# Kernel optimization log

Hardware: AMD Instinct MI355X
Metric: run time of the kernel (lower is better)

The kernel has to match this reference:

```python
import jax, jax.numpy as jnp
import numpy as np

# Wrapped module: Linear(2048->8192) + ReLU + Linear(8192->2048), both with bias.
D_IN, D_FF, D_OUT = 2048, 8192, 2048
N_W1 = D_FF * D_IN
N_B1 = D_FF
N_W2 = D_OUT * D_FF
N_B2 = D_OUT
NUM_WANDB = N_W1 + N_B1 + N_W2 + N_B2  # 33,564,672
SIZE_N = 5794  # ceil(sqrt(NUM_WANDB))
SIZE_M = 2897  # ceil(1.0 * SIZE_N / 2)
BATCH = 4096


def setup_inputs() -> dict:
    key = jax.random.key(0)
    k1, k2, k3 = jax.random.split(key, 3)
    x = jax.random.normal(k1, (BATCH, D_IN), dtype=jnp.float32)
    # scale factors keep reconstructed weights in a sane numeric range
    V1 = jax.random.normal(k2, (SIZE_N, SIZE_M), dtype=jnp.float32) * 0.02
    V2 = jax.random.normal(k3, (SIZE_N, SIZE_M), dtype=jnp.float32) * 0.02
    return {"x": x, "V1": V1, "V2": V2}


def reference(x, V1, V2):
    # V = V1 @ V2^T, flattened row-major (matches torch .view(-1, 1))
    V = jnp.matmul(V1, V2.T).reshape(-1)
    # Vectorized equivalent of WandBtoV's per-element copy loop:
    # consecutive slices of V fill each weight/bias in named_modules order.
    o = 0
    W1 = V[o:o + N_W1].reshape(D_FF, D_IN); o += N_W1   # linear1.weight [out,in]
    b1 = V[o:o + N_B1]; o += N_B1                        # linear1.bias
    W2 = V[o:o + N_W2].reshape(D_OUT, D_FF); o += N_W2   # linear2.weight
    b2 = V[o:o + N_B2]                                   # linear2.bias
    h = jax.nn.relu(jnp.matmul(x, W1.T) + b1)            # [B, D_FF]
    return jnp.matmul(h, W2.T) + b2                      # [B, D_OUT]
```

## Files before the change

### kernel.cpp

```cpp
#include <hip/hip_runtime.h>
#include <hip/hip_bf16.h>

typedef __attribute__((ext_vector_type(8))) __bf16 bf16x8;
typedef __attribute__((ext_vector_type(4))) __bf16 bf16x4;
typedef __attribute__((ext_vector_type(16))) float f32x16;

#define D_IN   2048
#define D_FF   8192
#define D_OUT  2048
#define BATCH  4096
#define SIZE_N 5794
#define SIZE_M 2897
#define PN 5888
#define PK 2944

#define OFF_B1 16777216
#define OFF_W2 16785408
#define OFF_B2 33562624

#define BK   32
#define NBUF 4

__device__ __forceinline__ void gload_lds16(const __bf16* g, __bf16* lds) {
    __builtin_amdgcn_global_load_lds(
        (const __attribute__((address_space(1))) void*)g,
        (__attribute__((address_space(3))) void*)lds,
        16, 0, 0);
}

template<int N> __device__ __forceinline__ void wait_vmcnt() {
    static_assert(N == 0 || N == 3 || N == 4 || N == 6 || N == 8, "unsupported vmcnt");
    if constexpr (N == 0)      asm volatile("s_waitcnt vmcnt(0)" ::: "memory");
    else if constexpr (N == 3) asm volatile("s_waitcnt vmcnt(3)" ::: "memory");
    else if constexpr (N == 4) asm volatile("s_waitcnt vmcnt(4)" ::: "memory");
    else if constexpr (N == 6) asm volatile("s_waitcnt vmcnt(6)" ::: "memory");
    else                       asm volatile("s_waitcnt vmcnt(8)" ::: "memory");
}
__device__ __forceinline__ void wait_lgkm0() {
    asm volatile("s_waitcnt lgkmcnt(0)" ::: "memory");
}

template<int MODE, int BM, int BN>
__global__ __launch_bounds__(512, 2)
void gemm_nt2(const __bf16* __restrict__ A, int lda,
              const __bf16* __restrict__ B, int ldb,
              void* __restrict__ Cv, int ldc,
              const __bf16* __restrict__ bias,
              int K, int Mvalid, int Nvalid)
{
    constexpr int LA = BM / 128;
    constexpr int LB = BN / 128;
    constexpr int L  = LA + LB;
    constexpr int FM = BM / 64;
    constexpr int FN = BN / 128;
    constexpr int ROWS = BM + BN;

    __shared__ bf16x8 lds[NBUF * ROWS * 4];

    const int tid  = threadIdx.x;
    const int wave = tid >> 6;
    const int lane = tid & 63;

    const int bm0 = blockIdx.x * BM;
    const int bn0 = blockIdx.y * BN;

    const int wm = wave >> 2;
    const int wn = wave & 3;

    const int srow   = lane >> 2;
    const int schunk = ((lane & 3) ^ ((lane >> 3) & 3)) * 8;

    const __bf16* aS = A + (size_t)(bm0 + wave * (BM / 8) + srow) * lda + schunk;
    const __bf16* bS = B + (size_t)(bn0 + wave * (BN / 8) + srow) * ldb + schunk;

    auto stage = [&](int t) {
        const int bb = t & (NBUF - 1);
        bf16x8* bufA = &lds[bb * ROWS * 4];
        bf16x8* bufB = bufA + BM * 4;
        const size_t kof = (size_t)t * BK;
        #pragma unroll
        for (int i = 0; i < LA; ++i)
            gload_lds16(aS + kof + (size_t)(16 * i) * lda,
                        (__bf16*)&bufA[(wave * (BM / 8) + 16 * i) * 4]);
        #pragma unroll
        for (int i = 0; i < LB; ++i)
            gload_lds16(bS + kof + (size_t)(16 * i) * ldb,
                        (__bf16*)&bufB[(wave * (BN / 8) + 16 * i) * 4]);
    };

    const int fr  = lane & 31;
    const int kh  = lane >> 5;
    const int swz = (fr >> 1) & 3;

    f32x16 acc[FM][FN] = {};

    const int nt = K / BK;

    stage(0); stage(1); stage(2);
    wait_vmcnt<2 * L>();
    __builtin_amdgcn_s_barrier();

    for (int t = 0; t < nt; ++t) {
        if (t + 3 < nt) stage(t + 3);

        const int bb = t & (NBUF - 1);
        const bf16x8* bufA = &lds[bb * ROWS * 4];
        const bf16x8* bufB = bufA + BM * 4;

        #pragma unroll
        for (int ks = 0; ks < 2; ++ks) {
            const int sl = (2 * ks + kh) ^ swz;
            bf16x8 af[FM], bq[FN];
            #pragma unroll
            for (int m = 0; m < FM; ++m)
                af[m] = bufA[(wm * (BM / 2) + m * 32 + fr) * 4 + sl];
            #pragma unroll
            for (int n = 0; n < FN; ++n)
                bq[n] = bufB[(wn * (BN / 4) + n * 32 + fr) * 4 + sl];
            __builtin_amdgcn_s_setprio(1);
            #pragma unroll
            for (int m = 0; m < FM; ++m) {
                #pragma unroll
                for (int n = 0; n < FN; ++n)
                    acc[m][n] = __builtin_amdgcn_mfma_f32_32x32x16_bf16(
                        af[m], bq[n], acc[m][n], 0, 0, 0);
            }
            __builtin_amdgcn_s_setprio(0);
        }

        if (t + 1 < nt) {
            wait_lgkm0();
            if      (t + 3 < nt) wait_vmcnt<2 * L>();
            else if (t + 2 < nt) wait_vmcnt<L>();
            else                 wait_vmcnt<0>();
            __builtin_amdgcn_s_barrier();
        }
    }

    const int ecol = lane & 31;
    const int er0  = 4 * kh;
    #pragma unroll
    for (int m = 0; m < FM; ++m) {
        #pragma unroll
        for (int n = 0; n < FN; ++n) {
            const int colBase = bn0 + wn * (BN / 4) + n * 32 + ecol;
            #pragma unroll
            for (int reg = 0; reg < 16; ++reg) {
                const int row = bm0 + wm * (BM / 2) + m * 32
                              + (reg & 3) + 8 * (reg >> 2) + er0;
                float v = acc[m][n][reg];
                if constexpr (MODE == 0) {
                    if (row < Mvalid && colBase < Nvalid)
                        ((__bf16*)Cv)[(size_t)row * ldc + colBase] = (__bf16)v;
                } else if constexpr (MODE == 1) {
                    v += (float)bias[colBase];
                    v = v > 0.f ? v : 0.f;
                    ((__bf16*)Cv)[(size_t)row * ldc + colBase] = (__bf16)v;
                } else {
                    v += (float)bias[colBase];
                    ((float*)Cv)[(size_t)row * ldc + colBase] = v;
                }
            }
        }
    }
}

__global__ void pad_cvt_bf16(const float* __restrict__ in, __bf16* __restrict__ out,
                             int rows, int cols, int pcols, int total)
{
    int idx = blockIdx.x * blockDim.x + threadIdx.x;
    if (idx >= total) return;
    int r = idx / pcols;
    int c = idx - r * pcols;
    float v = (r < rows && c < cols) ? in[(size_t)r * cols + c] : 0.0f;
    out[idx] = (__bf16)v;
}

__global__ void cvt_bf16_vec(const float4* __restrict__ in, bf16x4* __restrict__ out, int n4)
{
    int i = blockIdx.x * blockDim.x + threadIdx.x;
    if (i >= n4) return;
    float4 v = in[i];
    bf16x4 o;
    o.x = (__bf16)v.x; o.y = (__bf16)v.y; o.z = (__bf16)v.z; o.w = (__bf16)v.w;
    out[i] = o;
}

extern "C" void kernel_launch(void* const* d_in, const int* in_sizes, int n_in,
                              void* d_out, int out_size, void* d_ws, size_t ws_size,
                              hipStream_t stream)
{
    const float* x  = (const float*)d_in[0];
    const float* V1 = (const float*)d_in[1];
    const float* V2 = (const float*)d_in[2];
    float* out = (float*)d_out;

    char* ws = (char*)d_ws;
    const size_t vbElems  = (size_t)SIZE_N * SIZE_N;
    const size_t padElems = (size_t)PN * PK;

    size_t off = 0;
    __bf16* Vb = (__bf16*)(ws + off);
    off += ((vbElems * 2 + 255) / 256) * 256;
    __bf16* V1b = (__bf16*)(ws + off);
    __bf16* V2b = V1b + padElems;
    __bf16* hb  = (__bf16*)(ws + off);
    off += ((2 * padElems * 2 + 255) / 256) * 256;
    __bf16* xb = (__bf16*)(ws + off);
    off += (size_t)BATCH * D_IN * 2;
    if (ws_size < off) return;

    {
        int total  = (int)padElems;
        int blocks = (total + 255) / 256;
        pad_cvt_bf16<<<blocks, 256, 0, stream>>>(V1, V1b, SIZE_N, SIZE_M, PK, total);
        pad_cvt_bf16<<<blocks, 256, 0, stream>>>(V2, V2b, SIZE_N, SIZE_M, PK, total);
        int n4 = BATCH * D_IN / 4;
        cvt_bf16_vec<<<(n4 + 255) / 256, 256, 0, stream>>>((const float4*)x, (bf16x4*)xb, n4);
    }

    gemm_nt2<0, 256, 256><<<dim3(PN / 256, PN / 256), 512, 0, stream>>>(
        V1b, PK, V2b, PK, (void*)Vb, SIZE_N, (const __bf16*)nullptr, PK, SIZE_N, SIZE_N);

    gemm_nt2<1, 256, 256><<<dim3(BATCH / 256, D_FF / 256), 512, 0, stream>>>(
        xb, D_IN, Vb, D_IN, (void*)hb, D_FF, Vb + OFF_B1, D_IN, BATCH, D_FF);

    gemm_nt2<2, 128, 256><<<dim3(BATCH / 128, D_OUT / 256), 512, 0, stream>>>(
        hb, D_FF, Vb + OFF_W2, D_FF, (void*)out, D_OUT, Vb + OFF_B2, D_FF, BATCH, D_OUT);
}
```

Measured before the change: 780.0 us.

## Rework GEMM pipeline to 3-stage split A/B staging with smaller tiles

Replaces the GEMM kernel with a templated variant that uses a 3-buffer LDS ring. Loads for tile t+2 are interleaved: the A half is issued during the first k-substep and the B half during the second, with barriers around each MFMA block. Warp layout, thread count and occupancy become template parameters, and the three GEMMs switch to smaller 128x128 or 128x256 tiles with more blocks per CU. The aim is better latency hiding and occupancy, at the cost of more barriers per k-step and less data reuse per tile.

After: 813.2 us. 4.3% more time.

```diff
diff --git a/kernel.cpp b/kernel.cpp
--- a/kernel.cpp
+++ b/kernel.cpp
@@ -19,7 +19,7 @@
 #define OFF_B2 33562624
 
 #define BK   32
-#define NBUF 4
+#define NBUF 3
 
 __device__ __forceinline__ void gload_lds16(const __bf16* g, __bf16* lds) {
     __builtin_amdgcn_global_load_lds(
@@ -40,83 +40,91 @@
     asm volatile("s_waitcnt lgkmcnt(0)" ::: "memory");
 }
 
-template<int MODE, int BM, int BN>
-__global__ __launch_bounds__(512, 2)
-void gemm_nt2(const __bf16* __restrict__ A, int lda,
-              const __bf16* __restrict__ B, int ldb,
-              void* __restrict__ Cv, int ldc,
-              const __bf16* __restrict__ bias,
-              int K, int Mvalid, int Nvalid)
-{
-    constexpr int LA = BM / 128;
-    constexpr int LB = BN / 128;
-    constexpr int L  = LA + LB;
-    constexpr int FM = BM / 64;
-    constexpr int FN = BN / 128;
-    constexpr int ROWS = BM + BN;
-
-    __shared__ bf16x8 lds[NBUF * ROWS * 4];
+template<int MODE, int BM, int BN, int WM, int WN, int THREADS, int WEU>
+__global__ __launch_bounds__(THREADS, WEU)
+void gemm_p(const __bf16* __restrict__ A, int lda,
+            const __bf16* __restrict__ B, int ldb,
+            void* __restrict__ Cv, int ldc,
+            const __bf16* __restrict__ bias,
+            int K, int Mvalid, int Nvalid)
+{
+    constexpr int GA = (BM * 4) / THREADS;
+    constexpr int GB = (BN * 4) / THREADS;
+    constexpr int G  = GA + GB;
+    constexpr int FM = BM / (WM * 32);
+    constexpr int FN = BN / (WN * 32);
+    constexpr int TILE = (BM + BN) * 4;
+
+    __shared__ bf16x8 lds[NBUF * TILE];
 
     const int tid  = threadIdx.x;
     const int wave = tid >> 6;
     const int lane = tid & 63;
+    const int wm   = wave / WN;
+    const int wn   = wave % WN;
 
     const int bm0 = blockIdx.x * BM;
     const int bn0 = blockIdx.y * BN;
 
-    const int wm = wave >> 2;
-    const int wn = wave & 3;
-
-    const int srow   = lane >> 2;
-    const int schunk = ((lane & 3) ^ ((lane >> 3) & 3)) * 8;
-
-    const __bf16* aS = A + (size_t)(bm0 + wave * (BM / 8) + srow) * lda + schunk;
-    const __bf16* bS = B + (size_t)(bn0 + wave * (BN / 8) + srow) * ldb + schunk;
-
-    auto stage = [&](int t) {
-        const int bb = t & (NBUF - 1);
-        bf16x8* bufA = &lds[bb * ROWS * 4];
-        bf16x8* bufB = bufA + BM * 4;
+    const int srow   = tid >> 2;
+    const int schunk = ((tid & 3) ^ ((tid >> 3) & 3)) * 8;
+    const __bf16* aS = A + (size_t)(bm0 + srow) * lda + schunk;
+    const __bf16* bS = B + (size_t)(bn0 + srow) * ldb + schunk;
+
+    auto stageA = [&](bf16x8* buf, int t) {
         const size_t kof = (size_t)t * BK;
         #pragma unroll
-        for (int i = 0; i < LA; ++i)
-            gload_lds16(aS + kof + (size_t)(16 * i) * lda,
-                        (__bf16*)&bufA[(wave * (BM / 8) + 16 * i) * 4]);
-        #pragma unroll
-        for (int i = 0; i < LB; ++i)
-            gload_lds16(bS + kof + (size_t)(16 * i) * ldb,
-                        (__bf16*)&bufB[(wave * (BN / 8) + 16 * i) * 4]);
+        for (int g = 0; g < GA; ++g)
+            gload_lds16(aS + kof + (size_t)(g * (THREADS / 4)) * lda,
+                        (__bf16*)&buf[g * THREADS + tid]);
+    };
+    auto stageB = [&](bf16x8* buf, int t) {
+        const size_t kof = (size_t)t * BK;
+        #pragma unroll
+        for (int g = 0; g < GB; ++g)
+            gload_lds16(bS + kof + (size_t)(g * (THREADS / 4)) * ldb,
+                        (__bf16*)&buf[BM * 4 + g * THREADS + tid]);
     };
 
     const int fr  = lane & 31;
     const int kh  = lane >> 5;
-    const int swz = (fr >> 1) & 3;
+    const int sl0 = kh ^ ((fr >> 1) & 3);
+
+    int aOff[FM], bOff[FN];
+    #pragma unroll
+    for (int m = 0; m < FM; ++m) aOff[m] = (wm * (BM / WM) + m * 32 + fr) * 4;
+    #pragma unroll
+    for (int n = 0; n < FN; ++n) bOff[n] = (wn * (BN / WN) + n * 32 + fr) * 4;
 
     f32x16 acc[FM][FN] = {};
 
     const int nt = K / BK;
 
-    stage(0); stage(1); stage(2);
-    wait_vmcnt<2 * L>();
+    stageA(lds, 0);        stageB(lds, 0);
+    stageA(lds + TILE, 1); stageB(lds + TILE, 1);
+    wait_vmcnt<G>();
     __builtin_amdgcn_s_barrier();
 
+    int cur = 0, stg = 2;
     for (int t = 0; t < nt; ++t) {
-        if (t + 3 < nt) stage(t + 3);
-
-        const int bb = t & (NBUF - 1);
-        const bf16x8* bufA = &lds[bb * ROWS * 4];
-        const bf16x8* bufB = bufA + BM * 4;
-
+        bf16x8* bufA = lds + cur * TILE;
+        bf16x8* sbuf = lds + stg * TILE;
         #pragma unroll
         for (int ks = 0; ks < 2; ++ks) {
-            const int sl = (2 * ks + kh) ^ swz;
+            const int sl = sl0 ^ (ks << 1);
             bf16x8 af[FM], bq[FN];
             #pragma unroll
-            for (int m = 0; m < FM; ++m)
-                af[m] = bufA[(wm * (BM / 2) + m * 32 + fr) * 4 + sl];
-            #pragma unroll
-            for (int n = 0; n < FN; ++n)
-                bq[n] = bufB[(wn * (BN / 4) + n * 32 + fr) * 4 + sl];
+            for (int m = 0; m < FM; ++m) af[m] = bufA[aOff[m] + sl];
+            #pragma unroll
+            for (int n = 0; n < FN; ++n) bq[n] = bufA[BM * 4 + bOff[n] + sl];
+            if (t + 2 < nt) {
+                if (ks == 0) stageA(sbuf, t + 2);
+                else         stageB(sbuf, t + 2);
+            }
+            __builtin_amdgcn_sched_barrier(0);
+            __builtin_amdgcn_s_barrier();
+            wait_lgkm0();
+            __builtin_amdgcn_sched_barrier(0);
             __builtin_amdgcn_s_setprio(1);
             #pragma unroll
             for (int m = 0; m < FM; ++m) {
@@ -126,15 +134,16 @@
                         af[m], bq[n], acc[m][n], 0, 0, 0);
             }
             __builtin_amdgcn_s_setprio(0);
+            if (ks == 1 && t < nt - 1) {
+                if (t + 2 < nt) wait_vmcnt<G>();
+                else            wait_vmcnt<0>();
+            }
+            __builtin_amdgcn_sched_barrier(0);
+            if (!(ks == 1 && t == nt - 1))
+                __builtin_amdgcn_s_barrier();
         }
-
-        if (t + 1 < nt) {
-            wait_lgkm0();
-            if      (t + 3 < nt) wait_vmcnt<2 * L>();
-            else if (t + 2 < nt) wait_vmcnt<L>();
-            else                 wait_vmcnt<0>();
-            __builtin_amdgcn_s_barrier();
-        }
+        cur = (cur == NBUF - 1) ? 0 : cur + 1;
+        stg = (stg == NBUF - 1) ? 0 : stg + 1;
     }
 
     const int ecol = lane & 31;
@@ -143,10 +152,10 @@
     for (int m = 0; m < FM; ++m) {
         #pragma unroll
         for (int n = 0; n < FN; ++n) {
-            const int colBase = bn0 + wn * (BN / 4) + n * 32 + ecol;
+            const int colBase = bn0 + wn * (BN / WN) + n * 32 + ecol;
             #pragma unroll
             for (int reg = 0; reg < 16; ++reg) {
-                const int row = bm0 + wm * (BM / 2) + m * 32
+                const int row = bm0 + wm * (BM / WM) + m * 32
                               + (reg & 3) + 8 * (reg >> 2) + er0;
                 float v = acc[m][n][reg];
                 if constexpr (MODE == 0) {
@@ -219,12 +228,12 @@
         cvt_bf16_vec<<<(n4 + 255) / 256, 256, 0, stream>>>((const float4*)x, (bf16x4*)xb, n4);
     }
 
-    gemm_nt2<0, 256, 256><<<dim3(PN / 256, PN / 256), 512, 0, stream>>>(
+    gemm_p<0, 128, 128, 2, 2, 256, 3><<<dim3(PN / 128, PN / 128), 256, 0, stream>>>(
         V1b, PK, V2b, PK, (void*)Vb, SIZE_N, (const __bf16*)nullptr, PK, SIZE_N, SIZE_N);
 
-    gemm_nt2<1, 256, 256><<<dim3(BATCH / 256, D_FF / 256), 512, 0, stream>>>(
+    gemm_p<1, 128, 256, 2, 4, 512, 4><<<dim3(BATCH / 128, D_FF / 256), 512, 0, stream>>>(
         xb, D_IN, Vb, D_IN, (void*)hb, D_FF, Vb + OFF_B1, D_IN, BATCH, D_FF);
 
-    gemm_nt2<2, 128, 256><<<dim3(BATCH / 128, D_OUT / 256), 512, 0, stream>>>(
+    gemm_p<2, 128, 128, 2, 2, 256, 3><<<dim3(BATCH / 128, D_OUT / 128), 256, 0, stream>>>(
         hb, D_FF, Vb + OFF_W2, D_FF, (void*)out, D_OUT, Vb + OFF_B2, D_FF, BATCH, D_OUT);
 }
```

## Rewrite GEMM as 8-wave four-phase pipelined kernel with 16x16 MFMA and XCD swizzle

Applied to the files above, without the earlier changes.

Replaces the 4-buffer BK=32 GEMM, which used 32x32x16 MFMA, with a double-buffered BK=64 kernel. Each K step is split into four quadrant phases, and the global-to-LDS loads for the next tiles are interleaved between barrier-separated MFMA bursts. It uses 16x16x32 bf16 MFMA with XOR-swizzled LDS reads. The first GEMM also gets an XCD-aware block remapping to improve L2 locality. The aim is better overlap of memory traffic with compute, at the cost of larger LDS use per block and more barriers.

Result: faster. 746.8 us (-4.2%).

```diff
diff --git a/kernel.cpp b/kernel.cpp
--- a/kernel.cpp
+++ b/kernel.cpp
@@ -3,7 +3,7 @@
 
 typedef __attribute__((ext_vector_type(8))) __bf16 bf16x8;
 typedef __attribute__((ext_vector_type(4))) __bf16 bf16x4;
-typedef __attribute__((ext_vector_type(16))) float f32x16;
+typedef __attribute__((ext_vector_type(4))) float  f32x4;
 
 #define D_IN   2048
 #define D_FF   8192
@@ -18,151 +18,186 @@
 #define OFF_W2 16785408
 #define OFF_B2 33562624
 
-#define BK   32
-#define NBUF 4
-
-__device__ __forceinline__ void gload_lds16(const __bf16* g, __bf16* lds) {
+#define BK 64
+
+__device__ __forceinline__ void gload_lds16(const __bf16* g, __bf16* l) {
     __builtin_amdgcn_global_load_lds(
         (const __attribute__((address_space(1))) void*)g,
-        (__attribute__((address_space(3))) void*)lds,
-        16, 0, 0);
+        (__attribute__((address_space(3))) void*)l, 16, 0, 0);
 }
 
 template<int N> __device__ __forceinline__ void wait_vmcnt() {
-    static_assert(N == 0 || N == 3 || N == 4 || N == 6 || N == 8, "unsupported vmcnt");
+    static_assert(N==0 || N==2 || N==5 || N==6 || N==8, "unsupported vmcnt");
     if constexpr (N == 0)      asm volatile("s_waitcnt vmcnt(0)" ::: "memory");
-    else if constexpr (N == 3) asm volatile("s_waitcnt vmcnt(3)" ::: "memory");
-    else if constexpr (N == 4) asm volatile("s_waitcnt vmcnt(4)" ::: "memory");
+    else if constexpr (N == 2) asm volatile("s_waitcnt vmcnt(2)" ::: "memory");
+    else if constexpr (N == 5) asm volatile("s_waitcnt vmcnt(5)" ::: "memory");
     else if constexpr (N == 6) asm volatile("s_waitcnt vmcnt(6)" ::: "memory");
     else                       asm volatile("s_waitcnt vmcnt(8)" ::: "memory");
 }
-__device__ __forceinline__ void wait_lgkm0() {
-    asm volatile("s_waitcnt lgkmcnt(0)" ::: "memory");
-}
-
-template<int MODE, int BM, int BN>
+
+template<int NR>
+__device__ __forceinline__ void rdFrag(const __bf16* u, int row0, int kg, int sfl, bf16x8* F) {
+    #pragma unroll
+    for (int r = 0; r < NR; ++r)
+        #pragma unroll
+        for (int ks = 0; ks < 2; ++ks)
+            F[r * 2 + ks] = *(const bf16x8*)&u[(row0 + r * 16) * 64 + (((ks * 4 + kg) ^ sfl) * 8)];
+}
+
+template<int MQ, int NQ, int MH, int NH>
+__device__ __forceinline__ void mmq(const bf16x8* aF, const bf16x8* bF, f32x4 (*acc)[2 * NQ]) {
+    __builtin_amdgcn_s_setprio(1);
+    #pragma unroll
+    for (int ks = 0; ks < 2; ++ks)
+        #pragma unroll
+        for (int mq = 0; mq < MQ; ++mq)
+            #pragma unroll
+            for (int nq = 0; nq < NQ; ++nq)
+                acc[MH * MQ + mq][NH * NQ + nq] = __builtin_amdgcn_mfma_f32_16x16x32_bf16(
+                    aF[mq * 2 + ks], bF[nq * 2 + ks], acc[MH * MQ + mq][NH * NQ + nq], 0, 0, 0);
+    __builtin_amdgcn_s_setprio(0);
+}
+
+#define PH_MID() { __builtin_amdgcn_sched_barrier(0); __builtin_amdgcn_s_barrier(); \
+    asm volatile("s_waitcnt lgkmcnt(0)" ::: "memory"); __builtin_amdgcn_sched_barrier(0); }
+#define PH_END() { __builtin_amdgcn_sched_barrier(0); __builtin_amdgcn_s_barrier(); }
+
+template<int MODE, int BM, int BN, bool SWZ>
 __global__ __launch_bounds__(512, 2)
-void gemm_nt2(const __bf16* __restrict__ A, int lda,
-              const __bf16* __restrict__ B, int ldb,
-              void* __restrict__ Cv, int ldc,
-              const __bf16* __restrict__ bias,
-              int K, int Mvalid, int Nvalid)
-{
-    constexpr int LA = BM / 128;
-    constexpr int LB = BN / 128;
-    constexpr int L  = LA + LB;
-    constexpr int FM = BM / 64;
-    constexpr int FN = BN / 128;
-    constexpr int ROWS = BM + BN;
-
-    __shared__ bf16x8 lds[NBUF * ROWS * 4];
+void gemm8p(const __bf16* __restrict__ A, int lda,
+            const __bf16* __restrict__ B, int ldb,
+            void* __restrict__ Cv, int ldc,
+            const __bf16* __restrict__ bias,
+            int K, int Mvalid, int Nvalid)
+{
+    constexpr int RH = BM / 4,  CH = BN / 8;
+    constexpr int MQ = RH / 16, NQ = CH / 16;
+    constexpr int GA = BM / 128, GB = BN / 128;
+    constexpr int UA = BM * 32, UB = BN * 32;
+    constexpr int BUFE = 2 * UA + 2 * UB;
+    constexpr int W_P1 = 2 * (GA + GB);
+    constexpr int W_P3 = GA + 2 * GB;
+
+    __shared__ __bf16 lds[2 * BUFE];
 
     const int tid  = threadIdx.x;
     const int wave = tid >> 6;
     const int lane = tid & 63;
-
-    const int bm0 = blockIdx.x * BM;
-    const int bn0 = blockIdx.y * BN;
-
-    const int wm = wave >> 2;
-    const int wn = wave & 3;
-
-    const int srow   = lane >> 2;
-    const int schunk = ((lane & 3) ^ ((lane >> 3) & 3)) * 8;
-
-    const __bf16* aS = A + (size_t)(bm0 + wave * (BM / 8) + srow) * lda + schunk;
-    const __bf16* bS = B + (size_t)(bn0 + wave * (BN / 8) + srow) * ldb + schunk;
-
-    auto stage = [&](int t) {
-        const int bb = t & (NBUF - 1);
-        bf16x8* bufA = &lds[bb * ROWS * 4];
-        bf16x8* bufB = bufA + BM * 4;
-        const size_t kof = (size_t)t * BK;
-        #pragma unroll
-        for (int i = 0; i < LA; ++i)
-            gload_lds16(aS + kof + (size_t)(16 * i) * lda,
-                        (__bf16*)&bufA[(wave * (BM / 8) + 16 * i) * 4]);
-        #pragma unroll
-        for (int i = 0; i < LB; ++i)
-            gload_lds16(bS + kof + (size_t)(16 * i) * ldb,
-                        (__bf16*)&bufB[(wave * (BN / 8) + 16 * i) * 4]);
+    const int wm   = wave >> 2;
+    const int wn   = wave & 3;
+
+    int bx = blockIdx.x, by = blockIdx.y;
+    if constexpr (SWZ) {
+        const int nwg = gridDim.x * gridDim.y;
+        const int bid = by * gridDim.x + bx;
+        const int q = nwg >> 3, r = nwg & 7;
+        const int xcd = bid & 7, lid = bid >> 3;
+        const int nid = (xcd < r ? xcd * (q + 1) : r * (q + 1) + (xcd - r) * q) + lid;
+        bx = nid % gridDim.x;
+        by = nid / gridDim.x;
+    }
+    const int bm0 = bx * BM;
+    const int bn0 = by * BN;
+
+    const int srl = tid >> 3;
+    const int sch = ((tid & 7) ^ (srl & 7)) * 8;
+    const __bf16* Ab = A + sch;
+    const __bf16* Bb = B + sch;
+
+    auto stA = [&](int h, int pb, int t) {
+        #pragma unroll
+        for (int q = 0; q < GA; ++q) {
+            const int i = q * 64 + srl;
+            const int grow = bm0 + (i / RH) * (2 * RH) + h * RH + (i % RH);
+            gload_lds16(Ab + (size_t)grow * lda + (size_t)t * BK,
+                        &lds[pb * BUFE + h * UA + q * 4096 + wave * 512]);
+        }
     };
-
-    const int fr  = lane & 31;
-    const int kh  = lane >> 5;
-    const int swz = (fr >> 1) & 3;
-
-    f32x16 acc[FM][FN] = {};
+    auto stB = [&](int g, int pb, int t) {
+        #pragma unroll
+        for (int q = 0; q < GB; ++q) {
+            const int i = q * 64 + srl;
+            const int grow = bn0 + (i / CH) * (2 * CH) + g * CH + (i % CH);
+            gload_lds16(Bb + (size_t)grow * ldb + (size_t)t * BK,
+                        &lds[pb * BUFE + 2 * UA + g * UB + q * 4096 + wave * 512]);
+        }
+    };
+
+    const int fl   = lane & 15;
+    const int kg   = lane >> 4;
+    const int sfl  = fl & 7;
+    const int aRow = wm * RH + fl;
+    const int bRow = wn * CH + fl;
+
+    bf16x8 aF[2 * MQ], bF[2 * NQ];
+    f32x4  acc[2 * MQ][2 * NQ] = {};
 
     const int nt = K / BK;
 
-    stage(0); stage(1); stage(2);
-    wait_vmcnt<2 * L>();
+    stB(0, 0, 0); stA(1, 0, 0); stA(0, 0, 0); stB(1, 0, 0);
+    stB(0, 1, 1); stA(1, 1, 1);
+    wait_vmcnt<W_P3>();
     __builtin_amdgcn_s_barrier();
 
     for (int t = 0; t < nt; ++t) {
-        if (t + 3 < nt) stage(t + 3);
-
-        const int bb = t & (NBUF - 1);
-        const bf16x8* bufA = &lds[bb * ROWS * 4];
-        const bf16x8* bufB = bufA + BM * 4;
-
-        #pragma unroll
-        for (int ks = 0; ks < 2; ++ks) {
-            const int sl = (2 * ks + kh) ^ swz;
-            bf16x8 af[FM], bq[FN];
+        const int pc = t & 1, pn = pc ^ 1;
+        const __bf16* bufc = &lds[pc * BUFE];
+
+        if (t + 1 < nt) stA(0, pn, t + 1);
+        rdFrag<MQ>(bufc + 0 * UA,      aRow, kg, sfl, aF);
+        rdFrag<NQ>(bufc + 2 * UA,      bRow, kg, sfl, bF);
+        PH_MID();
+        mmq<MQ, NQ, 0, 0>(aF, bF, acc);
+        PH_END();
+
+        if (t + 1 < nt) stB(1, pn, t + 1);
+        rdFrag<MQ>(bufc + 1 * UA,      aRow, kg, sfl, aF);
+        PH_MID();
+        mmq<MQ, NQ, 1, 0>(aF, bF, acc);
+        if (t + 1 < nt) wait_vmcnt<W_P1>(); else wait_vmcnt<0>();
+        PH_END();
+
+        if (t + 2 < nt) stB(0, pc, t + 2);
+        rdFrag<NQ>(bufc + 2 * UA + UB, bRow, kg, sfl, bF);
+        PH_MID();
+        mmq<MQ, NQ, 1, 1>(aF, bF, acc);
+        PH_END();
+
+        if (t + 2 < nt) stA(1, pc, t + 2);
+        rdFrag<MQ>(bufc + 0 * UA,      aRow, kg, sfl, aF);
+        PH_MID();
+        mmq<MQ, NQ, 0, 1>(aF, bF, acc);
+        if (t + 1 < nt) { if (t + 2 < nt) wait_vmcnt<W_P3>(); else wait_vmcnt<2>(); }
+        PH_END();
+    }
+
+    const int er = kg * 4;
+    #pragma unroll
+    for (int mh = 0; mh < 2; ++mh)
+    #pragma unroll
+    for (int mq = 0; mq < MQ; ++mq)
+        #pragma unroll
+        for (int nh = 0; nh < 2; ++nh)
+        #pragma unroll
+        for (int nq = 0; nq < NQ; ++nq) {
+            const int col = bn0 + wn * (2 * CH) + nh * CH + nq * 16 + fl;
             #pragma unroll
-            for (int m = 0; m < FM; ++m)
-                af[m] = bufA[(wm * (BM / 2) + m * 32 + fr) * 4 + sl];
-            #pragma unroll
-            for (int n = 0; n < FN; ++n)
-                bq[n] = bufB[(wn * (BN / 4) + n * 32 + fr) * 4 + sl];
-            __builtin_amdgcn_s_setprio(1);
-            #pragma unroll
-            for (int m = 0; m < FM; ++m) {
-                #pragma unroll
-                for (int n = 0; n < FN; ++n)
-                    acc[m][n] = __builtin_amdgcn_mfma_f32_32x32x16_bf16(
-                        af[m], bq[n], acc[m][n], 0, 0, 0);
-            }
-            __builtin_amdgcn_s_setprio(0);
-        }
-
-        if (t + 1 < nt) {
-            wait_lgkm0();
-            if      (t + 3 < nt) wait_vmcnt<2 * L>();
-            else if (t + 2 < nt) wait_vmcnt<L>();
-            else                 wait_vmcnt<0>();
-            __builtin_amdgcn_s_barrier();
-        }
-    }
-
-    const int ecol = lane & 31;
-    const int er0  = 4 * kh;
-    #pragma unroll
-    for (int m = 0; m < FM; ++m) {
-        #pragma unroll
-        for (int n = 0; n < FN; ++n) {
-            const int colBase = bn0 + wn * (BN / 4) + n * 32 + ecol;
-            #pragma unroll
-            for (int reg = 0; reg < 16; ++reg) {
-                const int row = bm0 + wm * (BM / 2) + m * 32
-                              + (reg & 3) + 8 * (reg >> 2) + er0;
-                float v = acc[m][n][reg];
+            for (int reg = 0; reg < 4; ++reg) {
+                const int row = bm0 + wm * (2 * RH) + mh * RH + mq * 16 + er + reg;
+                float v = acc[mh * MQ + mq][nh * NQ + nq][reg];
                 if constexpr (MODE == 0) {
-                    if (row < Mvalid && colBase < Nvalid)
-                        ((__bf16*)Cv)[(size_t)row * ldc + colBase] = (__bf16)v;
+                    if (row < Mvalid && col < Nvalid)
+                        ((__bf16*)Cv)[(size_t)row * ldc + col] = (__bf16)v;
                 } else if constexpr (MODE == 1) {
-                    v += (float)bias[colBase];
+                    v += (float)bias[col];
                     v = v > 0.f ? v : 0.f;
-                    ((__bf16*)Cv)[(size_t)row * ldc + colBase] = (__bf16)v;
+                    ((__bf16*)Cv)[(size_t)row * ldc + col] = (__bf16)v;
                 } else {
-                    v += (float)bias[colBase];
-                    ((float*)Cv)[(size_t)row * ldc + colBase] = v;
+                    v += (float)bias[col];
+                    ((float*)Cv)[(size_t)row * ldc + col] = v;
                 }
             }
         }
-    }
 }
 
 __global__ void pad_cvt_bf16(const float* __restrict__ in, __bf16* __restrict__ out,
@@ -219,12 +254,12 @@
         cvt_bf16_vec<<<(n4 + 255) / 256, 256, 0, stream>>>((const float4*)x, (bf16x4*)xb, n4);
     }
 
-    gemm_nt2<0, 256, 256><<<dim3(PN / 256, PN / 256), 512, 0, stream>>>(
+    gemm8p<0, 256, 256, true><<<dim3(PN / 256, PN / 256), 512, 0, stream>>>(
         V1b, PK, V2b, PK, (void*)Vb, SIZE_N, (const __bf16*)nullptr, PK, SIZE_N, SIZE_N);
 
-    gemm_nt2<1, 256, 256><<<dim3(BATCH / 256, D_FF / 256), 512, 0, stream>>>(
+    gemm8p<1, 256, 256, false><<<dim3(BATCH / 256, D_FF / 256), 512, 0, stream>>>(
         xb, D_IN, Vb, D_IN, (void*)hb, D_FF, Vb + OFF_B1, D_IN, BATCH, D_FF);
 
-    gemm_nt2<2, 128, 256><<<dim3(BATCH / 128, D_OUT / 256), 512, 0, stream>>>(
+    gemm8p<2, 128, 256, false><<<dim3(BATCH / 128, D_OUT / 256), 512, 0, stream>>>(
         hb, D_FF, Vb + OFF_W2, D_FF, (void*)out, D_OUT, Vb + OFF_B2, D_FF, BATCH, D_OUT);
 }
```
